# Performance work log

Measured on AMD Instinct MI355X. Metric: run time of the kernel, lower is better.

Reference implementation:

```python
import jax, jax.numpy as jnp
import numpy as np

NUM_HEADS = 8
MASK_RATE = 0.5


def setup_inputs() -> dict:
    key = jax.random.key(0)
    ks = jax.random.split(key, 6)
    B, N, C = 8, 1024, 256
    TABLE = 10
    att_embedding = jax.random.normal(ks[0], (B, N, C), dtype=jnp.float32)
    relation_position = jax.random.randint(ks[1], (B, N, N), 0, TABLE, dtype=jnp.int32)
    rel_len = jax.random.randint(ks[2], (B,), 0, 20, dtype=jnp.int32)
    W_qkv = jax.random.normal(ks[3], (C, 3 * C), dtype=jnp.float32) * (1.0 / np.sqrt(C))
    W_proj = jax.random.normal(ks[4], (C, C), dtype=jnp.float32) * (1.0 / np.sqrt(C))
    b_proj = jnp.zeros((C,), dtype=jnp.float32)
    bias_table = jax.random.normal(ks[5], (TABLE, NUM_HEADS), dtype=jnp.float32) * 0.02
    return {
        "att_embedding": att_embedding,
        "relation_position": relation_position,
        "rel_len": rel_len,
        "W_qkv": W_qkv,
        "W_proj": W_proj,
        "b_proj": b_proj,
        "bias_table": bias_table,
    }


def reference(att_embedding, relation_position, rel_len, W_qkv, W_proj, b_proj, bias_table):
    B, N, C = att_embedding.shape
    H = NUM_HEADS
    hd = C // H
    scale = hd ** -0.5

    # QKV projection (no bias): [B,N,3C] -> q,k,v each [B,H,N,hd]
    qkv = (att_embedding @ W_qkv).reshape(B, N, 3, H, hd)
    qkv = jnp.transpose(qkv, (2, 0, 3, 1, 4))
    q, k, v = qkv[0], qkv[1], qkv[2]

    # Attention scores [B,H,N,N]
    attn = jnp.einsum("bhnd,bhmd->bhnm", q, k) * scale

    # Relative position bias: gather [B,N,N,H] -> [B,H,N,N]
    pos_bias = jnp.transpose(bias_table[relation_position], (0, 3, 1, 2))

    # Mask bias: table row t gets -100 iff t > mask_len (mask_len+1 .. TABLE-1);
    # identical across heads -> compute as [B,1,N,N] instead of materializing [B,H,N,N].
    mask_len = (rel_len.astype(jnp.float32) * MASK_RATE).astype(jnp.int32)
    mask_bias = jnp.where(relation_position > mask_len[:, None, None], -100.0, 0.0)[:, None]

    attn = jax.nn.softmax(attn + pos_bias + mask_bias, axis=-1)

    # Weighted values -> [B,N,C] -> output projection
    x = jnp.einsum("bhnm,bhmd->bnhd", attn, v).reshape(B, N, C)
    x = x @ W_proj + b_proj
    return x
```

## Files before the change

kernel.cpp:

```cpp
#include <hip/hip_runtime.h>
#include <hip/hip_bf16.h>

typedef __bf16 bf16;
typedef __bf16 bf16x2 __attribute__((ext_vector_type(2)));
typedef __bf16 bf16x8 __attribute__((ext_vector_type(8)));
typedef float f32x4 __attribute__((ext_vector_type(4)));
typedef int i32x4 __attribute__((ext_vector_type(4)));

#define B_ 8
#define N_ 1024
#define C_ 256
#define H_ 8
#define C3_ 768
#define SCALE 0.17677669529663689f
#define FMAX 16.0f


__global__ __launch_bounds__(256) void prep(
    const float* __restrict__ Wqkv, bf16* __restrict__ Wq_tiled)
{
  int o = blockIdx.x * 256 + threadIdx.x;
  int kk = o & 31;
  int idx = o >> 5;
  int nr = idx & 63;
  int qq = idx >> 6;
  int nt = qq % 12, kt = qq / 12;
  int n = nt * 64 + nr, k = kt * 32 + kk;
  Wq_tiled[o] = (bf16)Wqkv[k * C3_ + n];
}

__global__ __launch_bounds__(256) void gemm_qkv(
    const float* __restrict__ A, const bf16* __restrict__ Wq_tiled,
    const float* __restrict__ Wproj, const int* __restrict__ rel,
    bf16* __restrict__ q, bf16* __restrict__ kT, bf16* __restrict__ vT,
    bf16* __restrict__ Wp_tiled, unsigned char* __restrict__ rel8)
{
  __shared__ __align__(16) char sm[18432];

  int bb = blockIdx.x;
  int tid = threadIdx.x;

  if (bb >= 768) {
    if (bb < 2816) {
      long p = ((long)(bb - 768) * 256 + tid) * 16;
      i32x4 a = *reinterpret_cast<const i32x4*>(rel + p);
      i32x4 b2 = *reinterpret_cast<const i32x4*>(rel + p + 4);
      i32x4 c = *reinterpret_cast<const i32x4*>(rel + p + 8);
      i32x4 d = *reinterpret_cast<const i32x4*>(rel + p + 12);
      unsigned o0 = (unsigned)a[0] | ((unsigned)a[1] << 8) | ((unsigned)a[2] << 16) | ((unsigned)a[3] << 24);
      unsigned o1 = (unsigned)b2[0] | ((unsigned)b2[1] << 8) | ((unsigned)b2[2] << 16) | ((unsigned)b2[3] << 24);
      unsigned o2 = (unsigned)c[0] | ((unsigned)c[1] << 8) | ((unsigned)c[2] << 16) | ((unsigned)c[3] << 24);
      unsigned o3 = (unsigned)d[0] | ((unsigned)d[1] << 8) | ((unsigned)d[2] << 16) | ((unsigned)d[3] << 24);
      i32x4 ov = {(int)o0, (int)o1, (int)o2, (int)o3};
      *reinterpret_cast<i32x4*>(rel8 + p) = ov;
    } else {
      int p = (bb - 2816) * 256 + tid;
      int kk = p & 31;
      int n = (p >> 5) & 255;
      int kt = p >> 13;
      Wp_tiled[p] = (bf16)Wproj[(kt * 32 + kk) * C_ + n];
    }
    return;
  }

  bf16 (*As)[40] = (bf16(*)[40])(void*)sm;
  bf16 (*Bs)[40] = (bf16(*)[40])(void*)(sm + 5120);

  int wave = tid >> 6, lane = tid & 63, quad = lane >> 4, l16 = lane & 15;
  int x = bb & 127, y = bb >> 7;
  int m0 = x * 64, n0 = y * 128;
  int msub = (wave & 1) * 32, nsub = (wave >> 1) * 64;

  f32x4 acc[2][4] = {};

  int arow = tid >> 2, akc = (tid & 3) * 8;
  const float* aptr = A + (long)(m0 + arow) * C_ + akc;
  int bn = tid >> 1, bkc = (tid & 1) * 16;
  const bf16* bptr = Wq_tiled +
      ((long)(y * 2 + (bn >> 6)) * 2048 + (bn & 63) * 32 + bkc);

  float4 a0 = *reinterpret_cast<const float4*>(aptr);
  float4 a1 = *reinterpret_cast<const float4*>(aptr + 4);
  i32x4 bv0 = *reinterpret_cast<const i32x4*>(bptr);
  i32x4 bv1 = *reinterpret_cast<const i32x4*>(bptr + 8);

  for (int kt = 0; kt < 8; ++kt) {
    __syncthreads();
    {
      bf16 at[8] = {(bf16)a0.x, (bf16)a0.y, (bf16)a0.z, (bf16)a0.w,
                    (bf16)a1.x, (bf16)a1.y, (bf16)a1.z, (bf16)a1.w};
      *reinterpret_cast<bf16x8*>(&As[arow][akc]) = *reinterpret_cast<bf16x8*>(at);
      *reinterpret_cast<i32x4*>(&Bs[bn][bkc]) = bv0;
      *reinterpret_cast<i32x4*>(&Bs[bn][bkc + 8]) = bv1;
    }
    __syncthreads();

    if (kt < 7) {
      int kn = (kt + 1) * 32;
      a0 = *reinterpret_cast<const float4*>(aptr + kn);
      a1 = *reinterpret_cast<const float4*>(aptr + kn + 4);
      bv0 = *reinterpret_cast<const i32x4*>(bptr + (long)(kt + 1) * 24576);
      bv1 = *reinterpret_cast<const i32x4*>(bptr + (long)(kt + 1) * 24576 + 8);
    }

    bf16x8 af[2], bfr[4];
#pragma unroll
    for (int mi = 0; mi < 2; ++mi)
      af[mi] = *reinterpret_cast<const bf16x8*>(&As[msub + mi * 16 + l16][quad * 8]);
#pragma unroll
    for (int ni = 0; ni < 4; ++ni)
      bfr[ni] = *reinterpret_cast<const bf16x8*>(&Bs[nsub + ni * 16 + l16][quad * 8]);
#pragma unroll
    for (int mi = 0; mi < 2; ++mi)
#pragma unroll
      for (int ni = 0; ni < 4; ++ni)
        acc[mi][ni] = __builtin_amdgcn_mfma_f32_16x16x32_bf16(af[mi], bfr[ni], acc[mi][ni], 0, 0, 0);
  }

  __syncthreads();

  if (y < 4) {
    float mul = (y < 2) ? SCALE : 1.0f;
    bf16 (*Ep)[136] = (bf16(*)[136])(void*)sm;
#pragma unroll
    for (int mi = 0; mi < 2; ++mi)
#pragma unroll
      for (int ni = 0; ni < 4; ++ni)
#pragma unroll
        for (int r = 0; r < 4; ++r)
          Ep[msub + mi * 16 + quad * 4 + r][nsub + ni * 16 + l16] =
              (bf16)(acc[mi][ni][r] * mul);
    __syncthreads();
    int row = tid >> 2, seg = tid & 3;
    i32x4 w0 = *reinterpret_cast<const i32x4*>(&Ep[row][seg * 32]);
    i32x4 w1 = *reinterpret_cast<const i32x4*>(&Ep[row][seg * 32 + 8]);
    i32x4 w2 = *reinterpret_cast<const i32x4*>(&Ep[row][seg * 32 + 16]);
    i32x4 w3 = *reinterpret_cast<const i32x4*>(&Ep[row][seg * 32 + 24]);
    bf16* dst;
    if (y < 2) {
      dst = q + (long)(m0 + row) * 256 + n0 + seg * 32;
    } else {
      int c = n0 - 256 + seg * 32;
      int h = c >> 5;
      int gr = m0 + row, b = gr >> 10, n = gr & 1023;
      dst = kT + (((long)(b * H_ + h)) * N_ + n) * 32;
    }
    *reinterpret_cast<i32x4*>(dst) = w0;
    *reinterpret_cast<i32x4*>(dst + 8) = w1;
    *reinterpret_cast<i32x4*>(dst + 16) = w2;
    *reinterpret_cast<i32x4*>(dst + 24) = w3;
  } else {
    bf16 (*Vls)[72] = (bf16(*)[72])(void*)sm;
#pragma unroll
    for (int mi = 0; mi < 2; ++mi)
#pragma unroll
      for (int ni = 0; ni < 4; ++ni)
#pragma unroll
        for (int r = 0; r < 4; ++r) {
          int nn = msub + mi * 16 + quad * 4 + r;
          int np = (nn & ~31) | ((nn & 12) << 1) | (nn & 3) | (((nn >> 4) & 1) << 2);
          Vls[nsub + ni * 16 + l16][np] = (bf16)acc[mi][ni][r];
        }
    __syncthreads();
    int c = tid >> 1, nseg = (tid & 1) * 32;
    i32x4 w0 = *reinterpret_cast<const i32x4*>(&Vls[c][nseg]);
    i32x4 w1 = *reinterpret_cast<const i32x4*>(&Vls[c][nseg + 8]);
    i32x4 w2 = *reinterpret_cast<const i32x4*>(&Vls[c][nseg + 16]);
    i32x4 w3 = *reinterpret_cast<const i32x4*>(&Vls[c][nseg + 24]);
    int gb = m0 >> 10, mn = m0 & 1023;
    bf16* dst = vT + ((long)(gb * C_ + n0 - 512 + c)) * N_ + mn + nseg;
    *reinterpret_cast<i32x4*>(dst) = w0;
    *reinterpret_cast<i32x4*>(dst + 8) = w1;
    *reinterpret_cast<i32x4*>(dst + 16) = w2;
    *reinterpret_cast<i32x4*>(dst + 24) = w3;
  }
}

__global__ __launch_bounds__(512) void flash_attn(
    const bf16* __restrict__ q, const bf16* __restrict__ kT,
    const bf16* __restrict__ vT, const unsigned char* __restrict__ rel8,
    const int* __restrict__ rel_len, const float* __restrict__ btab,
    const bf16* __restrict__ Wp_tiled, const float* __restrict__ bias,
    float* __restrict__ out)
{
  __shared__ __align__(16) char smem[78336];
  char* const KB0 = smem;
  char* const VB0 = smem + 32768;
  char* const RB0 = smem + 65536;
  float* const ebtl = (float*)(smem + 77824);

  int tid = threadIdx.x;
  int h = tid >> 6, lane = tid & 63, quad = lane >> 4, l16 = lane & 15;

  int wg = blockIdx.y * 64 + blockIdx.x;
  int swz = (wg & 7) * 64 + (wg >> 3);
  int b = swz >> 6, i0 = (swz & 63) * 16;
  long bN = (long)b * N_;

  int mask_len = (int)((float)rel_len[b] * 0.5f);
  if (tid < 80) {
    int t = tid >> 3, hh = tid & 7;
    ebtl[hh * 16 + t] = __expf(btab[t * H_ + hh] + (t > mask_len ? -100.f : 0.f) - FMAX);
  }

  bf16x8 qf = *reinterpret_cast<const bf16x8*>(
      q + (bN + i0 + l16) * 256 + h * 32 + quad * 8);

  __syncthreads();

  int l = lane;
  int sxc = (((l & 3) ^ ((l >> 3) & 3)) << 4);
  int kc0 = (l >> 2) * 64 + sxc;
  int vc0 = (h * 32 + (l >> 2)) * 2048 + sxc;
  int rc0 = (l >> 3) * 1024 + (l & 7) * 4;

  const char* kTb = (const char*)kT + ((long)(b * 8 + h) << 16);
  const char* vTb = (const char*)vT + (long)b * 524288;
  const char* rb8 = (const char*)rel8 + (bN + i0) * 1024;

  int swq = ((quad ^ ((l16 >> 1) & 3)) << 4);
  int kr = h * 2048 + l16 * 64 + swq;
  int rr = h * 512 + l16 * 32 + quad * 4;

#define KB(i) (KB0 + (i) * 16384)
#define VB(i) (VB0 + (i) * 16384)
#define RB(i) (RB0 + (i) * 4096)

#define GLD16(G, L) __builtin_amdgcn_global_load_lds(                         \
    (const __attribute__((address_space(1))) void*)(G),                       \
    (__attribute__((address_space(3))) void*)(L), 16, 0, 0)
#define GLD4(G, L) __builtin_amdgcn_global_load_lds(                          \
    (const __attribute__((address_space(1))) void*)(G),                       \
    (__attribute__((address_space(3))) void*)(L), 4, 0, 0)

#define GATH(G, RV0, RV1) do {                                                \
    _Pragma("unroll")                                                         \
    for (int e = 0; e < 4; ++e) {                                             \
      G[e]     = ebtl[h * 16 + (int)((RV0 >> (8 * e)) & 255u)];               \
      G[4 + e] = ebtl[h * 16 + (int)((RV1 >> (8 * e)) & 255u)];               \
    }                                                                         \
  } while (0)

#define COMP(K0, K1, V0, V1, G) do {                                          \
    f32x4 z = {};                                                             \
    f32x4 s0 = __builtin_amdgcn_mfma_f32_16x16x32_bf16(K0, qf, z, 0, 0, 0);   \
    f32x4 s1 = __builtin_amdgcn_mfma_f32_16x16x32_bf16(K1, qf, z, 0, 0, 0);   \
    bf16x8 pa;                                                                \
    _Pragma("unroll")                                                         \
    for (int e = 0; e < 4; ++e) {                                             \
      float p0 = __expf(s0[e]) * G[e];                                        \
      float p1 = __expf(s1[e]) * G[4 + e];                                    \
      l_acc += p0 + p1;                                                       \
      pa[e] = (bf16)p0;                                                       \
      pa[4 + e] = (bf16)p1;                                                   \
    }                                                                         \
    oacc[0] = __builtin_amdgcn_mfma_f32_16x16x32_bf16(pa, V0, oacc[0], 0, 0, 0); \
    oacc[1] = __builtin_amdgcn_mfma_f32_16x16x32_bf16(pa, V1, oacc[1], 0, 0, 0); \
  } while (0)

#define TILE(T_, KVR, KVW, RR_, RW_, GC, GN) do {                             \
    int tn_ = ((T_) + 1) & 31, tr_ = ((T_) + 3) & 31;                         \
    GLD16(kTb + tn_ * 2048 + kc0,        KB(KVW) + h * 2048);                 \
    GLD16(kTb + tn_ * 2048 + kc0 + 1024, KB(KVW) + h * 2048 + 1024);          \
    GLD16(vTb + tn_ * 64 + vc0,          VB(KVW) + h * 2048);                 \
    GLD16(vTb + tn_ * 64 + vc0 + 32768,  VB(KVW) + h * 2048 + 1024);          \
    GLD4(rb8 + tr_ * 32 + rc0,           RB(RW_) + h * 512);                  \
    GLD4(rb8 + tr_ * 32 + rc0 + 8192,    RB(RW_) + h * 512 + 256);            \
    asm volatile("s_waitcnt vmcnt(8)" ::: "memory");                          \
    bf16x8 kf0 = *(const bf16x8*)(KB(KVR) + kr);                              \
    bf16x8 kf1 = *(const bf16x8*)(KB(KVR) + kr + 1024);                       \
    bf16x8 vf0 = *(const bf16x8*)(VB(KVR) + kr);                              \
    bf16x8 vf1 = *(const bf16x8*)(VB(KVR) + kr + 1024);                       \
    unsigned rv0 = *(const unsigned*)(RB(RR_) + rr);                          \
    unsigned rv1 = *(const unsigned*)(RB(RR_) + rr + 16);                     \
    GATH(GN, rv0, rv1);                                                       \
    COMP(kf0, kf1, vf0, vf1, GC);                                             \
  } while (0)

  f32x4 oacc[2] = {};
  float l_acc = 0.f;
  float gA[8], gB[8];

  GLD16(kTb + kc0,        KB(0) + h * 2048);
  GLD16(kTb + kc0 + 1024, KB(0) + h * 2048 + 1024);
  GLD16(vTb + vc0,          VB(0) + h * 2048);
  GLD16(vTb + vc0 + 32768,  VB(0) + h * 2048 + 1024);
  GLD4(rb8 + rc0,             RB(0) + h * 512);
  GLD4(rb8 + rc0 + 8192,      RB(0) + h * 512 + 256);
  GLD4(rb8 + 32 + rc0,        RB(1) + h * 512);
  GLD4(rb8 + 32 + rc0 + 8192, RB(1) + h * 512 + 256);
  GLD4(rb8 + 64 + rc0,        RB(2) + h * 512);
  GLD4(rb8 + 64 + rc0 + 8192, RB(2) + h * 512 + 256);
  asm volatile("s_waitcnt vmcnt(0)" ::: "memory");
  {
    unsigned rv0 = *(const unsigned*)(RB(0) + rr);
    unsigned rv1 = *(const unsigned*)(RB(0) + rr + 16);
    GATH(gA, rv0, rv1);
  }

#pragma unroll 1
  for (int t = 0; t < 30; t += 6) {
    TILE(t + 0, 0, 1, 1, 0, gA, gB);
    TILE(t + 1, 1, 0, 2, 1, gB, gA);
    TILE(t + 2, 0, 1, 0, 2, gA, gB);
    TILE(t + 3, 1, 0, 1, 0, gB, gA);
    TILE(t + 4, 0, 1, 2, 1, gA, gB);
    TILE(t + 5, 1, 0, 0, 2, gB, gA);
  }
  TILE(30, 0, 1, 1, 0, gA, gB);
  TILE(31, 1, 0, 2, 1, gB, gA);
#undef TILE
#undef COMP
#undef GATH
#undef GLD16
#undef GLD4
#undef KB
#undef VB
#undef RB

  asm volatile("s_waitcnt vmcnt(0)" ::: "memory");
  __syncthreads();

  float lsum = l_acc;
  lsum += __shfl_xor(lsum, 16);
  lsum += __shfl_xor(lsum, 32);
  float inv = 1.f / lsum;

  bf16 (*attL)[264] = (bf16(*)[264])(void*)smem;
#pragma unroll
  for (int r = 0; r < 4; ++r) {
    float invr = __shfl(inv, quad * 4 + r);
    attL[quad * 4 + r][h * 32 + l16] = (bf16)(oacc[0][r] * invr);
    attL[quad * 4 + r][h * 32 + 16 + l16] = (bf16)(oacc[1][r] * invr);
  }
  __syncthreads();

  f32x4 pacc[2] = {};
  const bf16* wp = Wp_tiled + ((h * 32 + l16) * 32 + quad * 8);
#pragma unroll
  for (int kt = 0; kt < 8; ++kt) {
    bf16x8 afr = *reinterpret_cast<const bf16x8*>(&attL[l16][kt * 32 + quad * 8]);
    bf16x8 b0 = *reinterpret_cast<const bf16x8*>(wp + kt * 8192);
    bf16x8 b1 = *reinterpret_cast<const bf16x8*>(wp + kt * 8192 + 512);
    pacc[0] = __builtin_amdgcn_mfma_f32_16x16x32_bf16(afr, b0, pacc[0], 0, 0, 0);
    pacc[1] = __builtin_amdgcn_mfma_f32_16x16x32_bf16(afr, b1, pacc[1], 0, 0, 0);
  }
  float bi0 = bias[h * 32 + l16];
  float bi1 = bias[h * 32 + 16 + l16];
#pragma unroll
  for (int r = 0; r < 4; ++r) {
    long rowoff = (bN + i0 + quad * 4 + r) * C_ + h * 32;
    out[rowoff + l16] = pacc[0][r] + bi0;
    out[rowoff + 16 + l16] = pacc[1][r] + bi1;
  }
}

extern "C" void kernel_launch(void* const* d_in, const int* in_sizes, int n_in,
                              void* d_out, int out_size, void* d_ws, size_t ws_size,
                              hipStream_t stream) {
  const float* X     = (const float*)d_in[0];
  const int*   rel   = (const int*)d_in[1];
  const int*   rlen  = (const int*)d_in[2];
  const float* Wqkv  = (const float*)d_in[3];
  const float* Wproj = (const float*)d_in[4];
  const float* bproj = (const float*)d_in[5];
  const float* btab  = (const float*)d_in[6];
  float* out = (float*)d_out;

  char* ws = (char*)d_ws;
  bf16* Wq_tiled = (bf16*)ws;
  bf16* Wp_tiled = (bf16*)(ws + 393216);
  bf16* q  = (bf16*)(ws + 524288);
  bf16* kT = (bf16*)(ws + 524288 + 4194304);
  bf16* vT = (bf16*)(ws + 524288 + 2 * 4194304);
  unsigned char* rel8 = (unsigned char*)(ws + 13107200);

  prep<<<dim3(768), 256, 0, stream>>>(Wqkv, Wq_tiled);
  gemm_qkv<<<dim3(3072), 256, 0, stream>>>(X, Wq_tiled, Wproj, rel,
                                           q, kT, vT, Wp_tiled, rel8);
  flash_attn<<<dim3(N_ / 16, B_), 512, 0, stream>>>(
      q, kT, vT, rel8, rlen, btab, Wp_tiled, bproj, out);
}
```

Before: 138.8 us.

## Load full-K QKV tiles into LDS, drop weight prep kernel, split side work

The QKV GEMM now loads the whole K=256 slice of A and W into LDS at once (135 KB of shared memory), converting fp32 weights to bf16 on the fly. This removes the separate weight-tiling prep kernel and the per-k-step barriers. Output tiles grow to 128x128, and the block index is remapped for locality. The rel8 packing and Wproj tiling move into a separate 'side' kernel launched after the GEMM. Each GEMM block now does more work and the grid is much smaller (384 blocks). The large LDS footprint limits occupancy to one block per CU, and the load phase is no longer overlapped with compute.

```diff
diff --git a/kernel.cpp b/kernel.cpp
--- a/kernel.cpp
+++ b/kernel.cpp
@@ -3,6 +3,7 @@
 
 typedef __bf16 bf16;
 typedef __bf16 bf16x2 __attribute__((ext_vector_type(2)));
+typedef __bf16 bf16x4 __attribute__((ext_vector_type(4)));
 typedef __bf16 bf16x8 __attribute__((ext_vector_type(8)));
 typedef float f32x4 __attribute__((ext_vector_type(4)));
 typedef int i32x4 __attribute__((ext_vector_type(4)));
@@ -16,102 +17,87 @@
 #define FMAX 16.0f
 
 
-__global__ __launch_bounds__(256) void prep(
-    const float* __restrict__ Wqkv, bf16* __restrict__ Wq_tiled)
-{
-  int o = blockIdx.x * 256 + threadIdx.x;
-  int kk = o & 31;
-  int idx = o >> 5;
-  int nr = idx & 63;
-  int qq = idx >> 6;
-  int nt = qq % 12, kt = qq / 12;
-  int n = nt * 64 + nr, k = kt * 32 + kk;
-  Wq_tiled[o] = (bf16)Wqkv[k * C3_ + n];
-}
-
-__global__ __launch_bounds__(256) void gemm_qkv(
-    const float* __restrict__ A, const bf16* __restrict__ Wq_tiled,
+__global__ __launch_bounds__(256) void side(
     const float* __restrict__ Wproj, const int* __restrict__ rel,
-    bf16* __restrict__ q, bf16* __restrict__ kT, bf16* __restrict__ vT,
     bf16* __restrict__ Wp_tiled, unsigned char* __restrict__ rel8)
 {
-  __shared__ __align__(16) char sm[18432];
-
   int bb = blockIdx.x;
   int tid = threadIdx.x;
-
-  if (bb >= 768) {
-    if (bb < 2816) {
-      long p = ((long)(bb - 768) * 256 + tid) * 16;
-      i32x4 a = *reinterpret_cast<const i32x4*>(rel + p);
-      i32x4 b2 = *reinterpret_cast<const i32x4*>(rel + p + 4);
-      i32x4 c = *reinterpret_cast<const i32x4*>(rel + p + 8);
-      i32x4 d = *reinterpret_cast<const i32x4*>(rel + p + 12);
-      unsigned o0 = (unsigned)a[0] | ((unsigned)a[1] << 8) | ((unsigned)a[2] << 16) | ((unsigned)a[3] << 24);
-      unsigned o1 = (unsigned)b2[0] | ((unsigned)b2[1] << 8) | ((unsigned)b2[2] << 16) | ((unsigned)b2[3] << 24);
-      unsigned o2 = (unsigned)c[0] | ((unsigned)c[1] << 8) | ((unsigned)c[2] << 16) | ((unsigned)c[3] << 24);
-      unsigned o3 = (unsigned)d[0] | ((unsigned)d[1] << 8) | ((unsigned)d[2] << 16) | ((unsigned)d[3] << 24);
-      i32x4 ov = {(int)o0, (int)o1, (int)o2, (int)o3};
-      *reinterpret_cast<i32x4*>(rel8 + p) = ov;
-    } else {
-      int p = (bb - 2816) * 256 + tid;
-      int kk = p & 31;
-      int n = (p >> 5) & 255;
-      int kt = p >> 13;
-      Wp_tiled[p] = (bf16)Wproj[(kt * 32 + kk) * C_ + n];
+  if (bb < 2048) {
+    long p = ((long)bb * 256 + tid) * 16;
+    i32x4 a = *reinterpret_cast<const i32x4*>(rel + p);
+    i32x4 b2 = *reinterpret_cast<const i32x4*>(rel + p + 4);
+    i32x4 c = *reinterpret_cast<const i32x4*>(rel + p + 8);
+    i32x4 d = *reinterpret_cast<const i32x4*>(rel + p + 12);
+    unsigned o0 = (unsigned)a[0] | ((unsigned)a[1] << 8) | ((unsigned)a[2] << 16) | ((unsigned)a[3] << 24);
+    unsigned o1 = (unsigned)b2[0] | ((unsigned)b2[1] << 8) | ((unsigned)b2[2] << 16) | ((unsigned)b2[3] << 24);
+    unsigned o2 = (unsigned)c[0] | ((unsigned)c[1] << 8) | ((unsigned)c[2] << 16) | ((unsigned)c[3] << 24);
+    unsigned o3 = (unsigned)d[0] | ((unsigned)d[1] << 8) | ((unsigned)d[2] << 16) | ((unsigned)d[3] << 24);
+    i32x4 ov = {(int)o0, (int)o1, (int)o2, (int)o3};
+    *reinterpret_cast<i32x4*>(rel8 + p) = ov;
+  } else {
+    int p = (bb - 2048) * 256 + tid;
+    int kk = p & 31;
+    int n = (p >> 5) & 255;
+    int kt = p >> 13;
+    Wp_tiled[p] = (bf16)Wproj[(kt * 32 + kk) * C_ + n];
+  }
+}
+
+__global__ __launch_bounds__(256) void gemm_qkv(
+    const float* __restrict__ A, const float* __restrict__ Wqkv,
+    bf16* __restrict__ q, bf16* __restrict__ kT, bf16* __restrict__ vT)
+{
+  __shared__ __align__(16) char sm[135168];
+  bf16 (*As)[264] = (bf16(*)[264])(void*)sm;
+  bf16 (*Bs)[264] = (bf16(*)[264])(void*)(sm + 67584);
+
+  int tid = threadIdx.x;
+  int wave = tid >> 6, lane = tid & 63, quad = lane >> 4, l16 = lane & 15;
+  int bb = blockIdx.x;
+  int y = bb >> 6;
+  int x = (bb & 7) * 8 + ((bb >> 3) & 7);
+  int m0 = x * 128, n0 = y * 128;
+  int msub = (wave & 1) * 64, nsub = (wave >> 1) * 64;
+
+  {
+    int ac = (tid & 63) * 4;
+    int ar0 = tid >> 6;
+#pragma unroll 4
+    for (int rr = 0; rr < 32; ++rr) {
+      int row = ar0 + rr * 4;
+      float4 f = *reinterpret_cast<const float4*>(A + (long)(m0 + row) * C_ + ac);
+      bf16x4 t = {(bf16)f.x, (bf16)f.y, (bf16)f.z, (bf16)f.w};
+      *reinterpret_cast<bf16x4*>(&As[row][ac]) = t;
     }
-    return;
-  }
-
-  bf16 (*As)[40] = (bf16(*)[40])(void*)sm;
-  bf16 (*Bs)[40] = (bf16(*)[40])(void*)(sm + 5120);
-
-  int wave = tid >> 6, lane = tid & 63, quad = lane >> 4, l16 = lane & 15;
-  int x = bb & 127, y = bb >> 7;
-  int m0 = x * 64, n0 = y * 128;
-  int msub = (wave & 1) * 32, nsub = (wave >> 1) * 64;
-
-  f32x4 acc[2][4] = {};
-
-  int arow = tid >> 2, akc = (tid & 3) * 8;
-  const float* aptr = A + (long)(m0 + arow) * C_ + akc;
-  int bn = tid >> 1, bkc = (tid & 1) * 16;
-  const bf16* bptr = Wq_tiled +
-      ((long)(y * 2 + (bn >> 6)) * 2048 + (bn & 63) * 32 + bkc);
-
-  float4 a0 = *reinterpret_cast<const float4*>(aptr);
-  float4 a1 = *reinterpret_cast<const float4*>(aptr + 4);
-  i32x4 bv0 = *reinterpret_cast<const i32x4*>(bptr);
-  i32x4 bv1 = *reinterpret_cast<const i32x4*>(bptr + 8);
-
+  }
+  {
+    int bn4 = (tid & 31) * 4;
+    int bk0 = tid >> 5;
+#pragma unroll 4
+    for (int kk = 0; kk < 32; ++kk) {
+      int k = bk0 + kk * 8;
+      float4 f = *reinterpret_cast<const float4*>(Wqkv + (long)k * C3_ + n0 + bn4);
+      Bs[bn4 + 0][k] = (bf16)f.x;
+      Bs[bn4 + 1][k] = (bf16)f.y;
+      Bs[bn4 + 2][k] = (bf16)f.z;
+      Bs[bn4 + 3][k] = (bf16)f.w;
+    }
+  }
+  __syncthreads();
+
+  f32x4 acc[4][4] = {};
+#pragma unroll
   for (int kt = 0; kt < 8; ++kt) {
-    __syncthreads();
-    {
-      bf16 at[8] = {(bf16)a0.x, (bf16)a0.y, (bf16)a0.z, (bf16)a0.w,
-                    (bf16)a1.x, (bf16)a1.y, (bf16)a1.z, (bf16)a1.w};
-      *reinterpret_cast<bf16x8*>(&As[arow][akc]) = *reinterpret_cast<bf16x8*>(at);
-      *reinterpret_cast<i32x4*>(&Bs[bn][bkc]) = bv0;
-      *reinterpret_cast<i32x4*>(&Bs[bn][bkc + 8]) = bv1;
-    }
-    __syncthreads();
-
-    if (kt < 7) {
-      int kn = (kt + 1) * 32;
-      a0 = *reinterpret_cast<const float4*>(aptr + kn);
-      a1 = *reinterpret_cast<const float4*>(aptr + kn + 4);
-      bv0 = *reinterpret_cast<const i32x4*>(bptr + (long)(kt + 1) * 24576);
-      bv1 = *reinterpret_cast<const i32x4*>(bptr + (long)(kt + 1) * 24576 + 8);
-    }
-
-    bf16x8 af[2], bfr[4];
-#pragma unroll
-    for (int mi = 0; mi < 2; ++mi)
-      af[mi] = *reinterpret_cast<const bf16x8*>(&As[msub + mi * 16 + l16][quad * 8]);
+    bf16x8 af[4], bfr[4];
+#pragma unroll
+    for (int mi = 0; mi < 4; ++mi)
+      af[mi] = *reinterpret_cast<const bf16x8*>(&As[msub + mi * 16 + l16][kt * 32 + quad * 8]);
 #pragma unroll
     for (int ni = 0; ni < 4; ++ni)
-      bfr[ni] = *reinterpret_cast<const bf16x8*>(&Bs[nsub + ni * 16 + l16][quad * 8]);
-#pragma unroll
-    for (int mi = 0; mi < 2; ++mi)
+      bfr[ni] = *reinterpret_cast<const bf16x8*>(&Bs[nsub + ni * 16 + l16][kt * 32 + quad * 8]);
+#pragma unroll
+    for (int mi = 0; mi < 4; ++mi)
 #pragma unroll
       for (int ni = 0; ni < 4; ++ni)
         acc[mi][ni] = __builtin_amdgcn_mfma_f32_16x16x32_bf16(af[mi], bfr[ni], acc[mi][ni], 0, 0, 0);
@@ -123,7 +109,7 @@
     float mul = (y < 2) ? SCALE : 1.0f;
     bf16 (*Ep)[136] = (bf16(*)[136])(void*)sm;
 #pragma unroll
-    for (int mi = 0; mi < 2; ++mi)
+    for (int mi = 0; mi < 4; ++mi)
 #pragma unroll
       for (int ni = 0; ni < 4; ++ni)
 #pragma unroll
@@ -131,28 +117,31 @@
           Ep[msub + mi * 16 + quad * 4 + r][nsub + ni * 16 + l16] =
               (bf16)(acc[mi][ni][r] * mul);
     __syncthreads();
-    int row = tid >> 2, seg = tid & 3;
-    i32x4 w0 = *reinterpret_cast<const i32x4*>(&Ep[row][seg * 32]);
-    i32x4 w1 = *reinterpret_cast<const i32x4*>(&Ep[row][seg * 32 + 8]);
-    i32x4 w2 = *reinterpret_cast<const i32x4*>(&Ep[row][seg * 32 + 16]);
-    i32x4 w3 = *reinterpret_cast<const i32x4*>(&Ep[row][seg * 32 + 24]);
-    bf16* dst;
-    if (y < 2) {
-      dst = q + (long)(m0 + row) * 256 + n0 + seg * 32;
-    } else {
-      int c = n0 - 256 + seg * 32;
-      int h = c >> 5;
-      int gr = m0 + row, b = gr >> 10, n = gr & 1023;
-      dst = kT + (((long)(b * H_ + h)) * N_ + n) * 32;
+#pragma unroll
+    for (int hh = 0; hh < 2; ++hh) {
+      int row = hh * 64 + (tid >> 2), seg = tid & 3;
+      i32x4 w0 = *reinterpret_cast<const i32x4*>(&Ep[row][seg * 32]);
+      i32x4 w1 = *reinterpret_cast<const i32x4*>(&Ep[row][seg * 32 + 8]);
+      i32x4 w2 = *reinterpret_cast<const i32x4*>(&Ep[row][seg * 32 + 16]);
+      i32x4 w3 = *reinterpret_cast<const i32x4*>(&Ep[row][seg * 32 + 24]);
+      bf16* dst;
+      if (y < 2) {
+        dst = q + (long)(m0 + row) * 256 + n0 + seg * 32;
+      } else {
+        int c = n0 - 256 + seg * 32;
+        int h = c >> 5;
+        int gr = m0 + row, b = gr >> 10, n = gr & 1023;
+        dst = kT + (((long)(b * H_ + h)) * N_ + n) * 32;
+      }
+      *reinterpret_cast<i32x4*>(dst) = w0;
+      *reinterpret_cast<i32x4*>(dst + 8) = w1;
+      *reinterpret_cast<i32x4*>(dst + 16) = w2;
+      *reinterpret_cast<i32x4*>(dst + 24) = w3;
     }
-    *reinterpret_cast<i32x4*>(dst) = w0;
-    *reinterpret_cast<i32x4*>(dst + 8) = w1;
-    *reinterpret_cast<i32x4*>(dst + 16) = w2;
-    *reinterpret_cast<i32x4*>(dst + 24) = w3;
   } else {
-    bf16 (*Vls)[72] = (bf16(*)[72])(void*)sm;
-#pragma unroll
-    for (int mi = 0; mi < 2; ++mi)
+    bf16 (*Vls)[136] = (bf16(*)[136])(void*)sm;
+#pragma unroll
+    for (int mi = 0; mi < 4; ++mi)
 #pragma unroll
       for (int ni = 0; ni < 4; ++ni)
 #pragma unroll
@@ -162,17 +151,13 @@
           Vls[nsub + ni * 16 + l16][np] = (bf16)acc[mi][ni][r];
         }
     __syncthreads();
-    int c = tid >> 1, nseg = (tid & 1) * 32;
-    i32x4 w0 = *reinterpret_cast<const i32x4*>(&Vls[c][nseg]);
-    i32x4 w1 = *reinterpret_cast<const i32x4*>(&Vls[c][nseg + 8]);
-    i32x4 w2 = *reinterpret_cast<const i32x4*>(&Vls[c][nseg + 16]);
-    i32x4 w3 = *reinterpret_cast<const i32x4*>(&Vls[c][nseg + 24]);
-    int gb = m0 >> 10, mn = m0 & 1023;
-    bf16* dst = vT + ((long)(gb * C_ + n0 - 512 + c)) * N_ + mn + nseg;
-    *reinterpret_cast<i32x4*>(dst) = w0;
-    *reinterpret_cast<i32x4*>(dst + 8) = w1;
-    *reinterpret_cast<i32x4*>(dst + 16) = w2;
-    *reinterpret_cast<i32x4*>(dst + 24) = w3;
+    int c = tid >> 1, nseg = (tid & 1) * 64;
+    int gb = x >> 3, mn = (x & 7) * 128;
+    bf16* dst = vT + ((long)(gb * C_ + (n0 - 512) + c)) * N_ + mn + nseg;
+#pragma unroll
+    for (int j = 0; j < 8; ++j)
+      *reinterpret_cast<i32x4*>(dst + j * 8) =
+          *reinterpret_cast<const i32x4*>(&Vls[c][nseg + j * 8]);
   }
 }
 
@@ -368,16 +353,14 @@
   float* out = (float*)d_out;
 
   char* ws = (char*)d_ws;
-  bf16* Wq_tiled = (bf16*)ws;
   bf16* Wp_tiled = (bf16*)(ws + 393216);
   bf16* q  = (bf16*)(ws + 524288);
   bf16* kT = (bf16*)(ws + 524288 + 4194304);
   bf16* vT = (bf16*)(ws + 524288 + 2 * 4194304);
   unsigned char* rel8 = (unsigned char*)(ws + 13107200);
 
-  prep<<<dim3(768), 256, 0, stream>>>(Wqkv, Wq_tiled);
-  gemm_qkv<<<dim3(3072), 256, 0, stream>>>(X, Wq_tiled, Wproj, rel,
-                                           q, kT, vT, Wp_tiled, rel8);
+  gemm_qkv<<<dim3(384), 256, 0, stream>>>(X, Wqkv, q, kT, vT);
+  side<<<dim3(2304), 256, 0, stream>>>(Wproj, rel, Wp_tiled, rel8);
   flash_attn<<<dim3(N_ / 16, B_), 512, 0, stream>>>(
       q, kT, vT, rel8, rlen, btab, Wp_tiled, bproj, out);
 }
```

Measured after the change: 155.6 us. +12.1%, slower.
